# Optimization experiments

Measured on AMD Instinct MI355X. Metric: run time of the kernel, lower is better.

## Reference

```python
import jax, jax.numpy as jnp
import numpy as np

B, N, C_IN, C_OUT, F = 8, 2048, 256, 256, 8
EPS = 1e-4

def setup_inputs() -> dict:
    key = jax.random.key(0)
    k1, k2, k3, k4, k5 = jax.random.split(key, 5)
    node_feats = jax.random.normal(k1, (B, N, C_IN), dtype=jnp.float32)
    # sparse-ish 0/1 adjacency with self-loops already added (as module assumes)
    adj = (jax.random.uniform(k2, (B, N, N)) < 0.02).astype(jnp.float32)
    eye = jnp.eye(N, dtype=jnp.float32)[None, :, :]
    adj_matrix = jnp.maximum(adj, eye)
    filters = jax.random.normal(k3, (F, C_OUT, C_IN), dtype=jnp.float32) * (1.0 / np.sqrt(C_IN))
    proj_w = jax.random.normal(k4, (1, F), dtype=jnp.float32) * (1.0 / np.sqrt(F))
    proj_b = jax.random.normal(k5, (1,), dtype=jnp.float32) * 0.01
    return {"node_feats": node_feats, "adj_matrix": adj_matrix,
            "filters": filters, "proj_w": proj_w, "proj_b": proj_b}

def reference(node_feats, adj_matrix, filters, proj_w, proj_b):
    # Multi-head filter transform + projection over heads, fused algebraically:
    # torch: ext[b,n,k,f] = sum_i filters[f,k,i]*x[b,n,i]; x' = ext @ proj_w.T + proj_b
    x = jnp.einsum('bni,fki,f->bnk', node_feats, filters, proj_w[0]) + proj_b[0]  # [B,N,c_out]
    # adjacency-weighted aggregation + mean normalization
    num_neighbours = jnp.sum(adj_matrix, axis=-1, keepdims=True)  # [B,N,1]
    agg = jnp.einsum('bij,bjk->bik', adj_matrix, x)  # [B,N,c_out]
    return agg / (num_neighbours + EPS)
```

## Files before the change

kernel.cpp:

```cpp
#include <hip/hip_runtime.h>
#include <hip/hip_bf16.h>

#define B_DIM  8
#define N_DIM  2048
#define CIN    256
#define COUT   256
#define F_DIM  8
#define EPS    1e-4f
#define CAP    128

using short8 = __attribute__((ext_vector_type(8))) short;
using f32x4  = __attribute__((ext_vector_type(4))) float;

__device__ __forceinline__ unsigned short f2bf(float f) {
    union { float f; unsigned u; } x; x.f = f;
    unsigned r = x.u + 0x7FFFu + ((x.u >> 16) & 1u);
    return (unsigned short)(r >> 16);
}
__device__ __forceinline__ float uf(unsigned u) {
    union { unsigned u; float f; } x; x.u = u;
    return x.f;
}

__global__ __launch_bounds__(256) void wb_build(const float* __restrict__ filters,
                                                const float* __restrict__ proj_w,
                                                unsigned short* __restrict__ Wb) {
    int gid = blockIdx.x * 256 + threadIdx.x;
    float acc = 0.f;
#pragma unroll
    for (int f = 0; f < F_DIM; ++f)
        acc += proj_w[f] * filters[f * (COUT * CIN) + gid];
    Wb[gid] = f2bf(acc);
}

__global__ __launch_bounds__(256) void xp_gemm(const float* __restrict__ nf,
                                               const unsigned short* __restrict__ Wb,
                                               const float* __restrict__ proj_b,
                                               unsigned short* __restrict__ xp) {
    const int tid  = threadIdx.x;
    const int lane = tid & 63;
    const int wv   = tid >> 6;
    const int m0   = blockIdx.x * 64;
    const int lrow = lane & 15;
    const int kgrp = lane >> 4;
    const float bias = proj_b[0];

    f32x4 acc[4][4];
#pragma unroll
    for (int a = 0; a < 4; ++a)
#pragma unroll
        for (int b = 0; b < 4; ++b)
            acc[a][b] = (f32x4){0.f, 0.f, 0.f, 0.f};

#pragma unroll
    for (int ks = 0; ks < 8; ++ks) {
        const int klane = ks * 32 + kgrp * 8;
        short8 af[4], bfr[4];
#pragma unroll
        for (int fm = 0; fm < 4; ++fm) {
            const float* ap = nf + (size_t)(m0 + fm * 16 + lrow) * CIN + klane;
            float4 a0 = *(const float4*)ap;
            float4 a1 = *(const float4*)(ap + 4);
            short8 t;
            t[0] = (short)f2bf(a0.x); t[1] = (short)f2bf(a0.y);
            t[2] = (short)f2bf(a0.z); t[3] = (short)f2bf(a0.w);
            t[4] = (short)f2bf(a1.x); t[5] = (short)f2bf(a1.y);
            t[6] = (short)f2bf(a1.z); t[7] = (short)f2bf(a1.w);
            af[fm] = t;
        }
#pragma unroll
        for (int fn = 0; fn < 4; ++fn) {
            const unsigned short* bp =
                Wb + (size_t)(wv * 64 + fn * 16 + lrow) * CIN + klane;
            bfr[fn] = *(const short8*)bp;
        }
#pragma unroll
        for (int fm = 0; fm < 4; ++fm)
#pragma unroll
            for (int fn = 0; fn < 4; ++fn)
                acc[fm][fn] = __builtin_amdgcn_mfma_f32_16x16x32_bf16(
                    af[fm], bfr[fn], acc[fm][fn], 0, 0, 0);
    }

#pragma unroll
    for (int fm = 0; fm < 4; ++fm)
#pragma unroll
        for (int fn = 0; fn < 4; ++fn) {
            const int gcol = wv * 64 + fn * 16 + lrow;
#pragma unroll
            for (int r = 0; r < 4; ++r) {
                const int grow = m0 + fm * 16 + kgrp * 4 + r;
                xp[(size_t)grow * COUT + gcol] = f2bf(acc[fm][fn][r] + bias);
            }
        }
}

__global__ __launch_bounds__(256) void csr_build(const float* __restrict__ adj,
                                                 unsigned short* __restrict__ idx,
                                                 int* __restrict__ cnt) {
    const int tid   = threadIdx.x;
    const int lane  = tid & 63;
    const int wid   = tid >> 6;
    const int bid   = blockIdx.x;
    const int b     = bid & 7;
    const int i     = (bid >> 3) * 4 + wid;
    const int row_g = b * N_DIM + i;

    const float* row = adj + (size_t)row_g * N_DIM;
    float4 v[8];
#pragma unroll
    for (int q = 0; q < 8; ++q)
        v[q] = *(const float4*)(row + q * 256 + lane * 4);

    unsigned nz = 0u;
#pragma unroll
    for (int q = 0; q < 8; ++q) {
        nz |= (v[q].x != 0.f ? 1u : 0u) << (4 * q + 0);
        nz |= (v[q].y != 0.f ? 1u : 0u) << (4 * q + 1);
        nz |= (v[q].z != 0.f ? 1u : 0u) << (4 * q + 2);
        nz |= (v[q].w != 0.f ? 1u : 0u) << (4 * q + 3);
    }
    const int c = __popc(nz);

    int pre = c;
#pragma unroll
    for (int off = 1; off < 64; off <<= 1) {
        int n = __shfl_up(pre, off, 64);
        if (lane >= off) pre += n;
    }
    const int total = __shfl(pre, 63, 64);

    int p = pre - c;
    unsigned m = nz;
    unsigned short* ib = idx + (size_t)row_g * CAP;
    while (m) {
        int e = __builtin_ctz(m);
        m &= m - 1;
        if (p < CAP)
            ib[p] = (unsigned short)(((e >> 2) << 8) + (lane << 2) + (e & 3));
        ++p;
    }
    if (lane == 63) cnt[row_g] = total;
}

__global__ __launch_bounds__(256) void csr_gather(const unsigned short* __restrict__ idx,
                                                  const int* __restrict__ cnt,
                                                  const unsigned short* __restrict__ xp,
                                                  float* __restrict__ out) {
    const int tid   = threadIdx.x;
    const int lane  = tid & 63;
    const int wid   = tid >> 6;
    const int bid   = blockIdx.x;
    const int b     = bid & 7;
    const int i     = (bid >> 3) * 4 + wid;
    const int row_g = b * N_DIM + i;

    const int ctrue = cnt[row_g];
    const int mcnt  = ctrue < CAP ? ctrue : CAP;
    const int h     = lane >> 5;
    const unsigned hsh = h * 16;

    const unsigned short* xb = xp + (size_t)b * (N_DIM * COUT) + (lane & 31) * 8;
    const unsigned short* ib = idx + (size_t)row_g * CAP;

    float a0=0.f,a1=0.f,a2=0.f,a3=0.f,a4=0.f,a5=0.f,a6=0.f,a7=0.f;

    for (int t = 0; t < mcnt; t += 16) {
        uint4 iv0 = *(const uint4*)(ib + t);
        uint4 iv1 = *(const uint4*)(ib + t + 8);
        unsigned w[8] = {iv0.x, iv0.y, iv0.z, iv0.w, iv1.x, iv1.y, iv1.z, iv1.w};
        uint4 g[8];
#pragma unroll
        for (int k = 0; k < 8; ++k) {
            int j = (int)((w[k] >> hsh) & 0xFFFFu) & (N_DIM - 1);
            g[k] = *(const uint4*)(xb + j * COUT);
        }
#pragma unroll
        for (int k = 0; k < 8; ++k) {
            const float s = (t + 2 * k + h) < mcnt ? 1.f : 0.f;
            a0 = fmaf(s, uf(g[k].x << 16),        a0);
            a1 = fmaf(s, uf(g[k].x & 0xFFFF0000u), a1);
            a2 = fmaf(s, uf(g[k].y << 16),        a2);
            a3 = fmaf(s, uf(g[k].y & 0xFFFF0000u), a3);
            a4 = fmaf(s, uf(g[k].z << 16),        a4);
            a5 = fmaf(s, uf(g[k].z & 0xFFFF0000u), a5);
            a6 = fmaf(s, uf(g[k].w << 16),        a6);
            a7 = fmaf(s, uf(g[k].w & 0xFFFF0000u), a7);
        }
    }

    a0 += __shfl_xor(a0, 32, 64); a1 += __shfl_xor(a1, 32, 64);
    a2 += __shfl_xor(a2, 32, 64); a3 += __shfl_xor(a3, 32, 64);
    a4 += __shfl_xor(a4, 32, 64); a5 += __shfl_xor(a5, 32, 64);
    a6 += __shfl_xor(a6, 32, 64); a7 += __shfl_xor(a7, 32, 64);

    const float inv = __builtin_amdgcn_rcpf((float)ctrue + EPS);
    if (lane < 32) {
        float* op = out + (size_t)row_g * COUT + lane * 8;
        float4 o0 = {a0 * inv, a1 * inv, a2 * inv, a3 * inv};
        float4 o1 = {a4 * inv, a5 * inv, a6 * inv, a7 * inv};
        *(float4*)op       = o0;
        *(float4*)(op + 4) = o1;
    }
}

extern "C" void kernel_launch(void* const* d_in, const int* in_sizes, int n_in,
                              void* d_out, int out_size, void* d_ws, size_t ws_size,
                              hipStream_t stream) {
    const float* nf      = (const float*)d_in[0];
    const float* adj     = (const float*)d_in[1];
    const float* filters = (const float*)d_in[2];
    const float* proj_w  = (const float*)d_in[3];
    const float* proj_b  = (const float*)d_in[4];
    float* out = (float*)d_out;

    char* ws = (char*)d_ws;
    unsigned short* Wb  = (unsigned short*)ws;
    unsigned short* xp  = (unsigned short*)(ws + 131072);
    int*            cnt = (int*)(ws + 131072 + 8388608);
    unsigned short* idx = (unsigned short*)(ws + 131072 + 8388608 + 65536);

    wb_build  <<<(COUT * CIN) / 256, 256, 0, stream>>>(filters, proj_w, Wb);
    xp_gemm   <<<(B_DIM * N_DIM) / 64, 256, 0, stream>>>(nf, Wb, proj_b, xp);
    csr_build <<<(B_DIM * N_DIM) / 4, 256, 0, stream>>>(adj, idx, cnt);
    csr_gather<<<(B_DIM * N_DIM) / 4, 256, 0, stream>>>(idx, cnt, xp, out);
}
```

Baseline: 69.42 us.

## Fuse CSR build and gather into one pipelined kernel with LDS index buffers

Merges the adjacency compaction kernel and the gather kernel into one kernel. Each wave handles 8 rows and prefetches the next row's adjacency data while it gathers the current row, with the compacted indices double-buffered in shared memory instead of global memory. This removes a launch and the global round trip for the index and count arrays, and lets the adjacency stream overlap the gathers. In exchange the grid drops to 512 blocks, which lowers parallelism and may cut the latency hiding available to the dense adjacency read.

```diff
diff --git a/kernel.cpp b/kernel.cpp
--- a/kernel.cpp
+++ b/kernel.cpp
@@ -95,113 +95,114 @@
         }
 }
 
-__global__ __launch_bounds__(256) void csr_build(const float* __restrict__ adj,
-                                                 unsigned short* __restrict__ idx,
-                                                 int* __restrict__ cnt) {
+__global__ __launch_bounds__(256) void agg_pipe(const float* __restrict__ adj,
+                                                const unsigned short* __restrict__ xp,
+                                                float* __restrict__ out) {
+    __shared__ __align__(16) unsigned short s_idx[4][2][CAP];
+
     const int tid   = threadIdx.x;
     const int lane  = tid & 63;
     const int wid   = tid >> 6;
     const int bid   = blockIdx.x;
     const int b     = bid & 7;
-    const int i     = (bid >> 3) * 4 + wid;
-    const int row_g = b * N_DIM + i;
-
-    const float* row = adj + (size_t)row_g * N_DIM;
-    float4 v[8];
-#pragma unroll
-    for (int q = 0; q < 8; ++q)
-        v[q] = *(const float4*)(row + q * 256 + lane * 4);
-
-    unsigned nz = 0u;
-#pragma unroll
-    for (int q = 0; q < 8; ++q) {
-        nz |= (v[q].x != 0.f ? 1u : 0u) << (4 * q + 0);
-        nz |= (v[q].y != 0.f ? 1u : 0u) << (4 * q + 1);
-        nz |= (v[q].z != 0.f ? 1u : 0u) << (4 * q + 2);
-        nz |= (v[q].w != 0.f ? 1u : 0u) << (4 * q + 3);
-    }
-    const int c = __popc(nz);
-
-    int pre = c;
-#pragma unroll
-    for (int off = 1; off < 64; off <<= 1) {
-        int n = __shfl_up(pre, off, 64);
-        if (lane >= off) pre += n;
-    }
-    const int total = __shfl(pre, 63, 64);
-
-    int p = pre - c;
-    unsigned m = nz;
-    unsigned short* ib = idx + (size_t)row_g * CAP;
-    while (m) {
-        int e = __builtin_ctz(m);
-        m &= m - 1;
-        if (p < CAP)
-            ib[p] = (unsigned short)(((e >> 2) << 8) + (lane << 2) + (e & 3));
-        ++p;
-    }
-    if (lane == 63) cnt[row_g] = total;
-}
-
-__global__ __launch_bounds__(256) void csr_gather(const unsigned short* __restrict__ idx,
-                                                  const int* __restrict__ cnt,
-                                                  const unsigned short* __restrict__ xp,
-                                                  float* __restrict__ out) {
-    const int tid   = threadIdx.x;
-    const int lane  = tid & 63;
-    const int wid   = tid >> 6;
-    const int bid   = blockIdx.x;
-    const int b     = bid & 7;
-    const int i     = (bid >> 3) * 4 + wid;
-    const int row_g = b * N_DIM + i;
-
-    const int ctrue = cnt[row_g];
-    const int mcnt  = ctrue < CAP ? ctrue : CAP;
+    const int rbase = (bid >> 3) * 32 + wid * 8;
     const int h     = lane >> 5;
     const unsigned hsh = h * 16;
 
+    const float* arow = adj + ((size_t)b * N_DIM + rbase) * N_DIM;
     const unsigned short* xb = xp + (size_t)b * (N_DIM * COUT) + (lane & 31) * 8;
-    const unsigned short* ib = idx + (size_t)row_g * CAP;
-
-    float a0=0.f,a1=0.f,a2=0.f,a3=0.f,a4=0.f,a5=0.f,a6=0.f,a7=0.f;
-
-    for (int t = 0; t < mcnt; t += 16) {
-        uint4 iv0 = *(const uint4*)(ib + t);
-        uint4 iv1 = *(const uint4*)(ib + t + 8);
-        unsigned w[8] = {iv0.x, iv0.y, iv0.z, iv0.w, iv1.x, iv1.y, iv1.z, iv1.w};
-        uint4 g[8];
-#pragma unroll
-        for (int k = 0; k < 8; ++k) {
-            int j = (int)((w[k] >> hsh) & 0xFFFFu) & (N_DIM - 1);
-            g[k] = *(const uint4*)(xb + j * COUT);
-        }
-#pragma unroll
-        for (int k = 0; k < 8; ++k) {
-            const float s = (t + 2 * k + h) < mcnt ? 1.f : 0.f;
-            a0 = fmaf(s, uf(g[k].x << 16),        a0);
-            a1 = fmaf(s, uf(g[k].x & 0xFFFF0000u), a1);
-            a2 = fmaf(s, uf(g[k].y << 16),        a2);
-            a3 = fmaf(s, uf(g[k].y & 0xFFFF0000u), a3);
-            a4 = fmaf(s, uf(g[k].z << 16),        a4);
-            a5 = fmaf(s, uf(g[k].z & 0xFFFF0000u), a5);
-            a6 = fmaf(s, uf(g[k].w << 16),        a6);
-            a7 = fmaf(s, uf(g[k].w & 0xFFFF0000u), a7);
-        }
+
+    float4 v[8];
+
+#define ISSUE(r)                                                     \
+    {                                                                \
+        const float* rp = arow + (size_t)(r) * N_DIM;                \
+        _Pragma("unroll")                                            \
+        for (int q = 0; q < 8; ++q)                                  \
+            v[q] = *(const float4*)(rp + q * 256 + lane * 4);        \
     }
 
-    a0 += __shfl_xor(a0, 32, 64); a1 += __shfl_xor(a1, 32, 64);
-    a2 += __shfl_xor(a2, 32, 64); a3 += __shfl_xor(a3, 32, 64);
-    a4 += __shfl_xor(a4, 32, 64); a5 += __shfl_xor(a5, 32, 64);
-    a6 += __shfl_xor(a6, 32, 64); a7 += __shfl_xor(a7, 32, 64);
-
-    const float inv = __builtin_amdgcn_rcpf((float)ctrue + EPS);
-    if (lane < 32) {
-        float* op = out + (size_t)row_g * COUT + lane * 8;
-        float4 o0 = {a0 * inv, a1 * inv, a2 * inv, a3 * inv};
-        float4 o1 = {a4 * inv, a5 * inv, a6 * inv, a7 * inv};
-        *(float4*)op       = o0;
-        *(float4*)(op + 4) = o1;
+    auto compact = [&](int par) -> int {
+        unsigned nz = 0u;
+#pragma unroll
+        for (int q = 0; q < 8; ++q) {
+            nz |= (v[q].x != 0.f ? 1u : 0u) << (4 * q + 0);
+            nz |= (v[q].y != 0.f ? 1u : 0u) << (4 * q + 1);
+            nz |= (v[q].z != 0.f ? 1u : 0u) << (4 * q + 2);
+            nz |= (v[q].w != 0.f ? 1u : 0u) << (4 * q + 3);
+        }
+        const int c = __popc(nz);
+        int pre = c;
+#pragma unroll
+        for (int off = 1; off < 64; off <<= 1) {
+            int n = __shfl_up(pre, off, 64);
+            if (lane >= off) pre += n;
+        }
+        const int total = __shfl(pre, 63, 64);
+        int p = pre - c;
+        unsigned m = nz;
+        unsigned short* ib = &s_idx[wid][par][0];
+        while (m) {
+            int e = __builtin_ctz(m);
+            m &= m - 1;
+            if (p < CAP)
+                ib[p] = (unsigned short)(((e >> 2) << 8) + (lane << 2) + (e & 3));
+            ++p;
+        }
+        return total;
+    };
+
+    ISSUE(0);
+    int cnt_cur = compact(0);
+
+    for (int r = 0; r < 8; ++r) {
+        if (r < 7) ISSUE(r + 1);
+
+        const int mcnt = cnt_cur < CAP ? cnt_cur : CAP;
+        const unsigned short* ib = &s_idx[wid][r & 1][0];
+        float a0=0.f,a1=0.f,a2=0.f,a3=0.f,a4=0.f,a5=0.f,a6=0.f,a7=0.f;
+
+        for (int t = 0; t < mcnt; t += 16) {
+            uint4 iv0 = *(const uint4*)(ib + t);
+            uint4 iv1 = *(const uint4*)(ib + t + 8);
+            unsigned w[8] = {iv0.x, iv0.y, iv0.z, iv0.w, iv1.x, iv1.y, iv1.z, iv1.w};
+            uint4 g[8];
+#pragma unroll
+            for (int k = 0; k < 8; ++k) {
+                int j = (int)((w[k] >> hsh) & 0xFFFFu) & (N_DIM - 1);
+                g[k] = *(const uint4*)(xb + j * COUT);
+            }
+#pragma unroll
+            for (int k = 0; k < 8; ++k) {
+                const float s = (t + 2 * k + h) < mcnt ? 1.f : 0.f;
+                a0 = fmaf(s, uf(g[k].x << 16),         a0);
+                a1 = fmaf(s, uf(g[k].x & 0xFFFF0000u), a1);
+                a2 = fmaf(s, uf(g[k].y << 16),         a2);
+                a3 = fmaf(s, uf(g[k].y & 0xFFFF0000u), a3);
+                a4 = fmaf(s, uf(g[k].z << 16),         a4);
+                a5 = fmaf(s, uf(g[k].z & 0xFFFF0000u), a5);
+                a6 = fmaf(s, uf(g[k].w << 16),         a6);
+                a7 = fmaf(s, uf(g[k].w & 0xFFFF0000u), a7);
+            }
+        }
+
+        a0 += __shfl_xor(a0, 32, 64); a1 += __shfl_xor(a1, 32, 64);
+        a2 += __shfl_xor(a2, 32, 64); a3 += __shfl_xor(a3, 32, 64);
+        a4 += __shfl_xor(a4, 32, 64); a5 += __shfl_xor(a5, 32, 64);
+        a6 += __shfl_xor(a6, 32, 64); a7 += __shfl_xor(a7, 32, 64);
+
+        const float inv = __builtin_amdgcn_rcpf((float)cnt_cur + EPS);
+        if (lane < 32) {
+            float* op = out + ((size_t)b * N_DIM + rbase + r) * COUT + lane * 8;
+            float4 o0 = {a0 * inv, a1 * inv, a2 * inv, a3 * inv};
+            float4 o1 = {a4 * inv, a5 * inv, a6 * inv, a7 * inv};
+            *(float4*)op       = o0;
+            *(float4*)(op + 4) = o1;
+        }
+
+        if (r < 7) cnt_cur = compact((r + 1) & 1);
     }
+#undef ISSUE
 }
 
 extern "C" void kernel_launch(void* const* d_in, const int* in_sizes, int n_in,
@@ -214,14 +215,10 @@
     const float* proj_b  = (const float*)d_in[4];
     float* out = (float*)d_out;
 
-    char* ws = (char*)d_ws;
-    unsigned short* Wb  = (unsigned short*)ws;
-    unsigned short* xp  = (unsigned short*)(ws + 131072);
-    int*            cnt = (int*)(ws + 131072 + 8388608);
-    unsigned short* idx = (unsigned short*)(ws + 131072 + 8388608 + 65536);
-
-    wb_build  <<<(COUT * CIN) / 256, 256, 0, stream>>>(filters, proj_w, Wb);
-    xp_gemm   <<<(B_DIM * N_DIM) / 64, 256, 0, stream>>>(nf, Wb, proj_b, xp);
-    csr_build <<<(B_DIM * N_DIM) / 4, 256, 0, stream>>>(adj, idx, cnt);
-    csr_gather<<<(B_DIM * N_DIM) / 4, 256, 0, stream>>>(idx, cnt, xp, out);
-}
+    unsigned short* Wb = (unsigned short*)d_ws;
+    unsigned short* xp = (unsigned short*)((char*)d_ws + 131072);
+
+    wb_build<<<(COUT * CIN) / 256, 256, 0, stream>>>(filters, proj_w, Wb);
+    xp_gemm <<<(B_DIM * N_DIM) / 64, 256, 0, stream>>>(nf, Wb, proj_b, xp);
+    agg_pipe<<<512, 256, 0, stream>>>(adj, xp, out);
+}
```

Measured after the change: 61.59 us. 1.13x faster.

## Split CSR gather into column slices with slice-major block ordering

Applied to the files above, without the earlier changes.

The gather kernel now splits the 256 output columns into four 64-column slices, with the slice index taken from the high bits of the block id, so the grid is four times larger. Each wave processes four neighbours per step across 16-lane groups with 8-byte loads, then reduces across groups with two xor-shuffles. Ordering blocks slice-major is meant to shrink the active working set of the bf16 projected features and raise cache hit rates. In exchange the index lists are read four times, per-lane loads are narrower, and more blocks must be launched.

```diff
diff --git a/kernel.cpp b/kernel.cpp
--- a/kernel.cpp
+++ b/kernel.cpp
@@ -143,64 +143,59 @@
     if (lane == 63) cnt[row_g] = total;
 }
 
-__global__ __launch_bounds__(256) void csr_gather(const unsigned short* __restrict__ idx,
-                                                  const int* __restrict__ cnt,
-                                                  const unsigned short* __restrict__ xp,
-                                                  float* __restrict__ out) {
+__global__ __launch_bounds__(256) void csr_gather4(const unsigned short* __restrict__ idx,
+                                                   const int* __restrict__ cnt,
+                                                   const unsigned short* __restrict__ xp,
+                                                   float* __restrict__ out) {
     const int tid   = threadIdx.x;
     const int lane  = tid & 63;
     const int wid   = tid >> 6;
     const int bid   = blockIdx.x;
-    const int b     = bid & 7;
-    const int i     = (bid >> 3) * 4 + wid;
-    const int row_g = b * N_DIM + i;
+    const int slice = bid >> 12;
+    const int rg    = bid & 4095;
+    const int row_g = rg * 4 + wid;
+    const int q     = lane >> 4;
+    const int cl    = lane & 15;
+    const int hi    = (q >> 1) & 1;
+    const unsigned sh = (q & 1) * 16;
 
     const int ctrue = cnt[row_g];
     const int mcnt  = ctrue < CAP ? ctrue : CAP;
-    const int h     = lane >> 5;
-    const unsigned hsh = h * 16;
-
-    const unsigned short* xb = xp + (size_t)b * (N_DIM * COUT) + (lane & 31) * 8;
+    const int b     = row_g >> 11;
     const unsigned short* ib = idx + (size_t)row_g * CAP;
-
-    float a0=0.f,a1=0.f,a2=0.f,a3=0.f,a4=0.f,a5=0.f,a6=0.f,a7=0.f;
-
-    for (int t = 0; t < mcnt; t += 16) {
-        uint4 iv0 = *(const uint4*)(ib + t);
-        uint4 iv1 = *(const uint4*)(ib + t + 8);
-        unsigned w[8] = {iv0.x, iv0.y, iv0.z, iv0.w, iv1.x, iv1.y, iv1.z, iv1.w};
-        uint4 g[8];
-#pragma unroll
-        for (int k = 0; k < 8; ++k) {
-            int j = (int)((w[k] >> hsh) & 0xFFFFu) & (N_DIM - 1);
-            g[k] = *(const uint4*)(xb + j * COUT);
-        }
-#pragma unroll
-        for (int k = 0; k < 8; ++k) {
-            const float s = (t + 2 * k + h) < mcnt ? 1.f : 0.f;
-            a0 = fmaf(s, uf(g[k].x << 16),        a0);
-            a1 = fmaf(s, uf(g[k].x & 0xFFFF0000u), a1);
-            a2 = fmaf(s, uf(g[k].y << 16),        a2);
-            a3 = fmaf(s, uf(g[k].y & 0xFFFF0000u), a3);
-            a4 = fmaf(s, uf(g[k].z << 16),        a4);
-            a5 = fmaf(s, uf(g[k].z & 0xFFFF0000u), a5);
-            a6 = fmaf(s, uf(g[k].w << 16),        a6);
-            a7 = fmaf(s, uf(g[k].w & 0xFFFF0000u), a7);
-        }
-    }
-
-    a0 += __shfl_xor(a0, 32, 64); a1 += __shfl_xor(a1, 32, 64);
-    a2 += __shfl_xor(a2, 32, 64); a3 += __shfl_xor(a3, 32, 64);
-    a4 += __shfl_xor(a4, 32, 64); a5 += __shfl_xor(a5, 32, 64);
-    a6 += __shfl_xor(a6, 32, 64); a7 += __shfl_xor(a7, 32, 64);
-
-    const float inv = __builtin_amdgcn_rcpf((float)ctrue + EPS);
-    if (lane < 32) {
-        float* op = out + (size_t)row_g * COUT + lane * 8;
-        float4 o0 = {a0 * inv, a1 * inv, a2 * inv, a3 * inv};
-        float4 o1 = {a4 * inv, a5 * inv, a6 * inv, a7 * inv};
-        *(float4*)op       = o0;
-        *(float4*)(op + 4) = o1;
+    const unsigned short* xb = xp + (size_t)b * (N_DIM * COUT) + slice * 64 + cl * 4;
+
+    float a0 = 0.f, a1 = 0.f, a2 = 0.f, a3 = 0.f;
+
+    for (int t = 0; t < mcnt; t += 8) {
+        uint4 uv = *(const uint4*)(ib + t);
+        unsigned w0 = hi ? uv.y : uv.x;
+        unsigned w1 = hi ? uv.w : uv.z;
+        const int j0 = (int)((w0 >> sh) & 0xFFFFu) & (N_DIM - 1);
+        const int j1 = (int)((w1 >> sh) & 0xFFFFu) & (N_DIM - 1);
+        uint2 g0 = *(const uint2*)(xb + (size_t)j0 * COUT);
+        uint2 g1 = *(const uint2*)(xb + (size_t)j1 * COUT);
+        const float s0 = (t + q) < mcnt ? 1.f : 0.f;
+        const float s1 = (t + q + 4) < mcnt ? 1.f : 0.f;
+        a0 = fmaf(s0, uf(g0.x << 16),         a0);
+        a1 = fmaf(s0, uf(g0.x & 0xFFFF0000u), a1);
+        a2 = fmaf(s0, uf(g0.y << 16),         a2);
+        a3 = fmaf(s0, uf(g0.y & 0xFFFF0000u), a3);
+        a0 = fmaf(s1, uf(g1.x << 16),         a0);
+        a1 = fmaf(s1, uf(g1.x & 0xFFFF0000u), a1);
+        a2 = fmaf(s1, uf(g1.y << 16),         a2);
+        a3 = fmaf(s1, uf(g1.y & 0xFFFF0000u), a3);
+    }
+
+    a0 += __shfl_xor(a0, 16, 64); a0 += __shfl_xor(a0, 32, 64);
+    a1 += __shfl_xor(a1, 16, 64); a1 += __shfl_xor(a1, 32, 64);
+    a2 += __shfl_xor(a2, 16, 64); a2 += __shfl_xor(a2, 32, 64);
+    a3 += __shfl_xor(a3, 16, 64); a3 += __shfl_xor(a3, 32, 64);
+
+    if (lane < 16) {
+        const float inv = __builtin_amdgcn_rcpf((float)ctrue + EPS);
+        float4 o = {a0 * inv, a1 * inv, a2 * inv, a3 * inv};
+        *(float4*)(out + (size_t)row_g * COUT + slice * 64 + cl * 4) = o;
     }
 }
 
@@ -220,8 +215,8 @@
     int*            cnt = (int*)(ws + 131072 + 8388608);
     unsigned short* idx = (unsigned short*)(ws + 131072 + 8388608 + 65536);
 
-    wb_build  <<<(COUT * CIN) / 256, 256, 0, stream>>>(filters, proj_w, Wb);
-    xp_gemm   <<<(B_DIM * N_DIM) / 64, 256, 0, stream>>>(nf, Wb, proj_b, xp);
-    csr_build <<<(B_DIM * N_DIM) / 4, 256, 0, stream>>>(adj, idx, cnt);
-    csr_gather<<<(B_DIM * N_DIM) / 4, 256, 0, stream>>>(idx, cnt, xp, out);
-}
+    wb_build   <<<(COUT * CIN) / 256, 256, 0, stream>>>(filters, proj_w, Wb);
+    xp_gemm    <<<(B_DIM * N_DIM) / 64, 256, 0, stream>>>(nf, Wb, proj_b, xp);
+    csr_build  <<<(B_DIM * N_DIM) / 4, 256, 0, stream>>>(adj, idx, cnt);
+    csr_gather4<<<4 * 4096, 256, 0, stream>>>(idx, cnt, xp, out);
+}
```

New measurement: 94.96 us. +36.8%, slower.
